# Kernel optimization log

Hardware: AMD Instinct MI355X
Metric: run time of the kernel (lower is better)

## Reference

```python
import jax, jax.numpy as jnp
import numpy as np

H, D, HID = 16, 128, 2048
B, S = 2, 2048
NUM_BLOCKS, BLOCK_SIZE = 32, 128


def _rope(x, cos, sin):
    # x: [T, H, D]; cos/sin: [T, D/2] (neox / rotate-half style)
    half = x.shape[-1] // 2
    x1, x2 = x[..., :half], x[..., half:]
    c = cos[:, None, :]
    s = sin[:, None, :]
    return jnp.concatenate([x1 * c - x2 * s, x2 * c + x1 * s], axis=-1)


def setup_inputs() -> dict:
    key = jax.random.key(0)
    ks = jax.random.split(key, 6)
    T = B * S
    hidden_states = jax.random.normal(ks[0], (T, HID), jnp.float32)
    wqkv = jax.random.normal(ks[1], (HID, 3 * HID), jnp.float32) * 0.02
    bqkv = jax.random.normal(ks[2], (3 * HID,), jnp.float32) * 0.02
    wo = jax.random.normal(ks[3], (HID, HID), jnp.float32) * 0.02
    # rotary tables, base 10000, dim = head_size
    inv_freq = 1.0 / (10000.0 ** (jnp.arange(0, D, 2, dtype=jnp.float32) / D))  # [D/2]
    pos = jnp.tile(jnp.arange(S, dtype=jnp.float32), B)  # positions per token [T]
    ang = pos[:, None] * inv_freq[None, :]  # [T, D/2]
    cos, sin = jnp.cos(ang), jnp.sin(ang)
    k_cache = jnp.zeros((NUM_BLOCKS, BLOCK_SIZE, H, D), jnp.float32)
    v_cache = jnp.zeros((NUM_BLOCKS, BLOCK_SIZE, H, D), jnp.float32)
    cu_seqlen_prefill = jnp.array([0, S, 2 * S], jnp.int32)
    slots = jnp.arange(T, dtype=jnp.int32)
    return {"hidden_states": hidden_states, "cos": cos, "sin": sin,
            "wqkv": wqkv, "bqkv": bqkv, "wo": wo,
            "k_cache": k_cache, "v_cache": v_cache,
            "cu_seqlen_prefill": cu_seqlen_prefill, "slots": slots, "max_s": S}


def reference(hidden_states, cos, sin, wqkv, bqkv, wo, k_cache, v_cache,
              cu_seqlen_prefill, slots, max_s):
    T = hidden_states.shape[0]
    # fused QKV projection (c_attn)
    qkv = hidden_states @ wqkv + bqkv  # [T, 3*H*D]
    q, k, v = jnp.split(qkv, [H * D, 2 * H * D], axis=1)
    q = q.reshape(T, H, D)
    k = k.reshape(T, H, D)
    v = v.reshape(T, H, D)
    # rotary embedding on q and k (in-place in torch; functional here)
    q = _rope(q, cos, sin)
    k = _rope(k, cos, sin)
    # reshape_and_cache: scatter post-rope k and v into paged KV cache by slot
    kc = k_cache.reshape(-1, H, D).at[slots].set(k).reshape(k_cache.shape)
    vc = v_cache.reshape(-1, H, D).at[slots].set(v).reshape(v_cache.shape)
    # prefill flash attention: varlen causal; equal-length sequences here
    b, s = T // max_s, max_s
    qb = q.reshape(b, s, H, D)
    kb = k.reshape(b, s, H, D)
    vb = v.reshape(b, s, H, D)
    scale = D ** -0.5
    scores = jnp.einsum('bqhd,bkhd->bhqk', qb, kb) * scale  # [B,H,S,S]
    causal = jnp.tril(jnp.ones((s, s), bool))
    scores = jnp.where(causal[None, None], scores, jnp.finfo(scores.dtype).min)
    probs = jax.nn.softmax(scores, axis=-1)
    attn = jnp.einsum('bhqk,bkhd->bqhd', probs, vb).reshape(T, H * D)
    out = attn @ wo  # c_proj, no bias
    return out, kc, vc
```

## Files before the change

kernel.cpp:

```cpp
#include <hip/hip_runtime.h>

using f32x4  = __attribute__((ext_vector_type(4))) float;
using frag16 = __attribute__((ext_vector_type(8))) short;
using s16x4  = __attribute__((ext_vector_type(4))) short;
using s16x8  = __attribute__((ext_vector_type(8))) short;
using u32x4  = __attribute__((ext_vector_type(4))) unsigned;

#define DI __device__ __forceinline__

constexpr int HID  = 2048;
constexpr int NH   = 16;
constexpr int HD   = 128;
constexpr int TT   = 4096;
constexpr int SEQ  = 2048;
constexpr int NQKV = 3 * HID;

DI short f2bf(float f) {
  unsigned u = __builtin_bit_cast(unsigned, f);
  unsigned r = (u + 0x7fffu + ((u >> 16) & 1u)) >> 16;
  return (short)r;
}
DI float bf2f(short s) {
  unsigned u = ((unsigned)(unsigned short)s) << 16;
  return __builtin_bit_cast(float, u);
}
DI unsigned cvtpk(float lo, float hi) {
  unsigned r;
  asm("v_cvt_pk_bf16_f32 %0, %1, %2" : "=v"(r) : "v"(lo), "v"(hi));
  return r;
}

struct alignas(8) S4h { short a, b, c, d; };

__global__ void conv_f32_bf16(const float* __restrict__ in, short* __restrict__ out) {
  int gid = blockIdx.x * 256 + threadIdx.x;
  const float4* in4 = (const float4*)in;
  float4 v = in4[gid];
  S4h o{f2bf(v.x), f2bf(v.y), f2bf(v.z), f2bf(v.w)};
  ((S4h*)out)[gid] = o;
}

template <bool IN_F32, bool PERM>
__global__ void transpose_conv(const void* __restrict__ in_, short* __restrict__ out,
                               int ldin, int R) {
  __shared__ float t[64][65];
  const float* inf = (const float*)in_;
  const short* ins = (const short*)in_;
  int tid = threadIdx.x;
  int bx = blockIdx.x, by = blockIdx.y;
#pragma unroll
  for (int i = 0; i < 4; i++) {
    int idx = i * 256 + tid;
    int r = idx >> 4, c4 = idx & 15;
    size_t gi = (size_t)(by * 64 + r) * ldin + bx * 64 + c4 * 4;
    if (IN_F32) {
      float4 v = *(const float4*)(inf + gi);
      t[r][c4 * 4] = v.x; t[r][c4 * 4 + 1] = v.y;
      t[r][c4 * 4 + 2] = v.z; t[r][c4 * 4 + 3] = v.w;
    } else {
      s16x4 v = *(const s16x4*)(ins + gi);
#pragma unroll
      for (int j = 0; j < 4; j++) t[r][c4 * 4 + j] = bf2f(v[j]);
    }
  }
  __syncthreads();
#pragma unroll
  for (int i = 0; i < 4; i++) {
    int idx = i * 256 + tid;
    int r = idx >> 4, c4 = idx & 15;
    s16x4 o;
#pragma unroll
    for (int j = 0; j < 4; j++) {
      int c = c4 * 4 + j;
      int cs = PERM ? (16 * (c & 3) + 4 * (c >> 4) + ((c >> 2) & 3)) : c;
      o[j] = f2bf(t[cs][r]);
    }
    *(s16x4*)(out + (size_t)(bx * 64 + r) * R + by * 64 + c4 * 4) = o;
  }
}

#define GLDS(src, dst)                                                     \
  __builtin_amdgcn_global_load_lds(                                        \
      (const __attribute__((address_space(1))) void*)(src),                \
      (__attribute__((address_space(3))) void*)(dst), 16, 0, 0)

template <bool ADD_BIAS, bool OUT_BF16>
__global__ __launch_bounds__(256, 2) void gemm_bt(
    const short* __restrict__ A, const short* __restrict__ Bt,
    const float* __restrict__ bias, void* __restrict__ Cout,
    int M, int N, int K) {
  __shared__ alignas(16) short Al[128 * 64];
  __shared__ alignas(16) short Bl[128 * 64];
  const int tid = threadIdx.x;
  const int wid = tid >> 6, lane = tid & 63;
  const int wr = wid >> 1, wc = wid & 1;
  const int l15 = lane & 15, lg = lane >> 4;
  const int gx = gridDim.x;
  const int id = blockIdx.y * gx + blockIdx.x;
  const int nwg = gx * gridDim.y;
  const int swz = (id & 7) * (nwg >> 3) + (id >> 3);
  const int row0 = (swz / gx) * 128, col0 = (swz % gx) * 128;
  const int lr8 = lane >> 3, l7 = lane & 7;

  f32x4 acc[4][4];
#pragma unroll
  for (int i = 0; i < 4; i++)
#pragma unroll
    for (int j = 0; j < 4; j++) acc[i][j] = {0.f, 0.f, 0.f, 0.f};

  for (int kt = 0; kt < K; kt += 64) {
#pragma unroll
    for (int c = 0; c < 4; c++) {
      int chunk = c * 4 + wid;
      int r = chunk * 8 + lr8;
      int ke = (l7 * 8) ^ ((r & 7) * 8);
      GLDS(A + (size_t)(row0 + r) * K + kt + ke, Al + chunk * 512);
      GLDS(Bt + (size_t)(col0 + r) * K + kt + ke, Bl + chunk * 512);
    }
    __syncthreads();
#pragma unroll
    for (int kk = 0; kk < 2; kk++) {
      frag16 af[4], bfv[4];
#pragma unroll
      for (int ai = 0; ai < 4; ai++) {
        int r = wr * 64 + ai * 16 + l15;
        int k0 = kk * 32 + lg * 8;
        af[ai] = *(const frag16*)(Al + r * 64 + (k0 ^ ((r & 7) * 8)));
      }
#pragma unroll
      for (int bj = 0; bj < 4; bj++) {
        int r = wc * 64 + bj * 16 + l15;
        int k0 = kk * 32 + lg * 8;
        bfv[bj] = *(const frag16*)(Bl + r * 64 + (k0 ^ ((r & 7) * 8)));
      }
#pragma unroll
      for (int ai = 0; ai < 4; ai++)
#pragma unroll
        for (int bj = 0; bj < 4; bj++)
          acc[ai][bj] = __builtin_amdgcn_mfma_f32_16x16x32_bf16(
              af[ai], bfv[bj], acc[ai][bj], 0, 0, 0);
    }
    __syncthreads();
  }
#pragma unroll
  for (int ai = 0; ai < 4; ai++) {
#pragma unroll
    for (int bj = 0; bj < 4; bj++) {
      int row = row0 + wr * 64 + ai * 16 + lg * 4;
      int col = col0 + wc * 64 + bj * 16 + l15;
      float bv = 0.f;
      if (ADD_BIAS) bv = bias[col];
#pragma unroll
      for (int r = 0; r < 4; r++) {
        float v = acc[ai][bj][r] + bv;
        if (OUT_BF16)
          ((short*)Cout)[(size_t)(row + r) * N + col] = f2bf(v);
        else
          ((float*)Cout)[(size_t)(row + r) * N + col] = v;
      }
    }
  }
}

__global__ void rope_scatter(const short* __restrict__ qkv, const float* __restrict__ cs,
                             const float* __restrict__ sn, const int* __restrict__ slots,
                             short* __restrict__ Qb, short* __restrict__ Kb,
                             float* __restrict__ kc, float* __restrict__ vc) {
  const float SCL = 0.08838834764831845f * 1.4426950408889634f;
  const int t = blockIdx.x;
  const int tid = threadIdx.x;
  const int slot = slots[t];
  const short* row = qkv + (size_t)t * NQKV;
  short* qo = Qb + (size_t)t * HID;
  short* ko = Kb + (size_t)t * HID;
  float* kco = kc + (size_t)slot * HID;
  float* vco = vc + (size_t)slot * HID;

  const int h = tid >> 4, d0 = (tid & 15) * 4;
  const int c1 = h * 128 + d0, c2 = c1 + 64;
  float4 c4 = *(const float4*)(cs + (size_t)t * 64 + d0);
  float4 s4 = *(const float4*)(sn + (size_t)t * 64 + d0);
  float cc[4] = {c4.x, c4.y, c4.z, c4.w};
  float ssv[4] = {s4.x, s4.y, s4.z, s4.w};
  s16x4 q1 = *(const s16x4*)(row + c1);
  s16x4 q2 = *(const s16x4*)(row + c2);
  s16x4 k1 = *(const s16x4*)(row + HID + c1);
  s16x4 k2 = *(const s16x4*)(row + HID + c2);
  s16x4 qo1, qo2, ko1, ko2;
  float kcv1[4], kcv2[4];
#pragma unroll
  for (int r = 0; r < 4; r++) {
    float a = bf2f(q1[r]), b = bf2f(q2[r]);
    qo1[r] = f2bf((a * cc[r] - b * ssv[r]) * SCL);
    qo2[r] = f2bf((b * cc[r] + a * ssv[r]) * SCL);
    float ka = bf2f(k1[r]), kb = bf2f(k2[r]);
    float o1 = ka * cc[r] - kb * ssv[r];
    float o2 = kb * cc[r] + ka * ssv[r];
    ko1[r] = f2bf(o1);
    ko2[r] = f2bf(o2);
    kcv1[r] = o1;
    kcv2[r] = o2;
  }
  *(s16x4*)(qo + c1) = qo1;
  *(s16x4*)(qo + c2) = qo2;
  *(s16x4*)(ko + c1) = ko1;
  *(s16x4*)(ko + c2) = ko2;
  *(float4*)(kco + c1) = {kcv1[0], kcv1[1], kcv1[2], kcv1[3]};
  *(float4*)(kco + c2) = {kcv2[0], kcv2[1], kcv2[2], kcv2[3]};

  const int vi = tid * 8;
  s16x8 v8 = *(const s16x8*)(row + 2 * HID + vi);
  *(float4*)(vco + vi)     = {bf2f(v8[0]), bf2f(v8[1]), bf2f(v8[2]), bf2f(v8[3])};
  *(float4*)(vco + vi + 4) = {bf2f(v8[4]), bf2f(v8[5]), bf2f(v8[6]), bf2f(v8[7])};
}

__global__ __launch_bounds__(256, 2) void flash_attn5(
    const short* __restrict__ Qb, const short* __restrict__ Kb,
    const short* __restrict__ Vt, short* __restrict__ attn) {
  __shared__ alignas(16) short Klds[2][64 * 128];
  __shared__ alignas(16) short Vlds[2][128 * 64];
  __shared__ alignas(16) short plds[4][16 * 72];

  const int tid = threadIdx.x;
  const int w = tid >> 6, lane = tid & 63;
  const int l15 = lane & 15, lg = lane >> 4;
  const int bid = blockIdx.x;
  const int p = bid >> 5;
  const int bh = bid & 31;
  const int b = bh >> 4, h = bh & 15;
  short* pl = &plds[w][0];

  frag16 ones;
#pragma unroll
  for (int j = 0; j < 8; j++) ones[j] = (short)0x3F80;

  auto stage = [&](int kv0, int buf) {
#pragma unroll
    for (int ci = 0; ci < 4; ci++) {
      int cc = w * 4 + ci;
      int krow = cc * 4 + (lane >> 4);
      int kss = (lane & 15) ^ (krow & 15);
      GLDS(Kb + (size_t)(b * SEQ + kv0 + krow) * HID + h * HD + kss * 8,
           Klds[buf] + cc * 512);
      int vd = cc * 8 + (lane >> 3);
      int vss = (lane & 7) ^ (vd & 7);
      GLDS(Vt + (size_t)(h * HD + vd) * TT + b * SEQ + kv0 + vss * 8,
           Vlds[buf] + cc * 512);
    }
  };

  const int qrowH = (31 - p) * 64 + w * 16;
  const int qrowL = p * 64 + w * 16;
  const int ntH = 32 - p;

  frag16 qfH[4], qfL[4];
  {
    const short* qpH = Qb + (size_t)(b * SEQ + qrowH + l15) * HID + h * HD + lg * 8;
    const short* qpL = Qb + (size_t)(b * SEQ + qrowL + l15) * HID + h * HD + lg * 8;
#pragma unroll
    for (int ds = 0; ds < 4; ds++) {
      qfH[ds] = *(const frag16*)(qpH + ds * 32);
      qfL[ds] = *(const frag16*)(qpL + ds * 32);
    }
  }
  f32x4 oH[8], oL[8];
#pragma unroll
  for (int j = 0; j < 8; j++) { oH[j] = {0.f, 0.f, 0.f, 0.f}; oL[j] = {0.f, 0.f, 0.f, 0.f}; }
  f32x4 laH = {0.f, 0.f, 0.f, 0.f}, laL = {0.f, 0.f, 0.f, 0.f};
  float mrH = -1e30f, mrL = -1e30f;

  auto proc = [&](const frag16 (&qf)[4], f32x4 (&o)[8], f32x4& la, float& mr,
                  bool diag, const short* Kl, const short* Vl) {
    f32x4 sa[4];
#pragma unroll
    for (int f = 0; f < 4; f++) sa[f] = {0.f, 0.f, 0.f, 0.f};
#pragma unroll
    for (int ds = 0; ds < 4; ds++) {
      int phys = (ds * 4 + lg) ^ l15;
#pragma unroll
      for (int f = 0; f < 4; f++) {
        frag16 kf = *(const frag16*)(Kl + (f * 16 + l15) * 128 + phys * 8);
        sa[f] = __builtin_amdgcn_mfma_f32_16x16x32_bf16(kf, qf[ds], sa[f], 0, 0, 0);
      }
    }
    if (diag) {
      int ql = 16 * w + l15;
#pragma unroll
      for (int f = 0; f < 4; f++)
#pragma unroll
        for (int r = 0; r < 4; r++)
          if (f * 16 + lg * 4 + r > ql) sa[f][r] = -1e30f;
    }
    float pm = sa[0][0];
#pragma unroll
    for (int f = 0; f < 4; f++)
#pragma unroll
      for (int r = 0; r < 4; r++) pm = fmaxf(pm, sa[f][r]);
    pm = fmaxf(pm, __shfl_xor(pm, 16));
    pm = fmaxf(pm, __shfl_xor(pm, 32));
    if (__any(pm > mr + 8.f)) {
      float mn = fmaxf(mr, pm);
      float frl = exp2f(mr - mn);
      mr = mn;
      float fr4[4];
#pragma unroll
      for (int r = 0; r < 4; r++)
        fr4[r] = __shfl(frl, lg * 16 + lg * 4 + r);
#pragma unroll
      for (int r = 0; r < 4; r++) {
        la[r] *= fr4[r];
#pragma unroll
        for (int j = 0; j < 8; j++) o[j][r] *= fr4[r];
      }
    }
    float pe[4][4];
#pragma unroll
    for (int f = 0; f < 4; f++)
#pragma unroll
      for (int r = 0; r < 4; r++) pe[f][r] = exp2f(sa[f][r] - mr);
    unsigned wv[8];
#pragma unroll
    for (int r = 0; r < 4; r++) {
      wv[2 * r]     = cvtpk(pe[0][r], pe[1][r]);
      wv[2 * r + 1] = cvtpk(pe[2][r], pe[3][r]);
    }
    {
      u32x4* pb = (u32x4*)(pl + l15 * 72 + lg * 16);
      pb[0] = {wv[0], wv[1], wv[2], wv[3]};
      pb[1] = {wv[4], wv[5], wv[6], wv[7]};
    }
    asm volatile("s_waitcnt lgkmcnt(0)" ::: "memory");
    frag16 pf0 = *(const frag16*)(pl + l15 * 72 + lg * 8);
    frag16 pf1 = *(const frag16*)(pl + l15 * 72 + 32 + lg * 8);
    la = __builtin_amdgcn_mfma_f32_16x16x32_bf16(pf0, ones, la, 0, 0, 0);
    la = __builtin_amdgcn_mfma_f32_16x16x32_bf16(pf1, ones, la, 0, 0, 0);
#pragma unroll
    for (int j = 0; j < 8; j++) {
      int d = j * 16 + l15;
      int p0 = lg ^ (d & 7);
      int p1 = (4 + lg) ^ (d & 7);
      frag16 vf0 = *(const frag16*)(Vl + d * 64 + p0 * 8);
      frag16 vf1 = *(const frag16*)(Vl + d * 64 + p1 * 8);
      o[j] = __builtin_amdgcn_mfma_f32_16x16x32_bf16(pf0, vf0, o[j], 0, 0, 0);
      o[j] = __builtin_amdgcn_mfma_f32_16x16x32_bf16(pf1, vf1, o[j], 0, 0, 0);
    }
  };

  stage(0, 0);
  __syncthreads();

  int cur = 0;
  for (int t = 0; t < ntH; t++) {
    if (t + 1 < ntH) stage((t + 1) * 64, cur ^ 1);
    const short* Kl = &Klds[cur][0];
    const short* Vl = &Vlds[cur][0];
    proc(qfH, oH, laH, mrH, t == ntH - 1, Kl, Vl);
    if (t <= p) proc(qfL, oL, laL, mrL, t == p, Kl, Vl);
    __syncthreads();
    cur ^= 1;
  }

  {
    float inv[4];
#pragma unroll
    for (int r = 0; r < 4; r++) inv[r] = 1.f / laH[r];
    short* op = attn + (size_t)(b * SEQ + qrowH + lg * 4) * HID + h * HD + l15;
#pragma unroll
    for (int j = 0; j < 8; j++)
#pragma unroll
      for (int r = 0; r < 4; r++)
        op[(size_t)r * HID + j * 16] = f2bf(oH[j][r] * inv[r]);
  }
  {
    float inv[4];
#pragma unroll
    for (int r = 0; r < 4; r++) inv[r] = 1.f / laL[r];
    short* op = attn + (size_t)(b * SEQ + qrowL + lg * 4) * HID + h * HD + l15;
#pragma unroll
    for (int j = 0; j < 8; j++)
#pragma unroll
      for (int r = 0; r < 4; r++)
        op[(size_t)r * HID + j * 16] = f2bf(oL[j][r] * inv[r]);
  }
}

extern "C" void kernel_launch(void* const* d_in, const int* in_sizes, int n_in,
                              void* d_out, int out_size, void* d_ws, size_t ws_size,
                              hipStream_t stream) {
  const float* hidden = (const float*)d_in[0];
  const float* cosb   = (const float*)d_in[1];
  const float* sinb   = (const float*)d_in[2];
  const float* wqkv   = (const float*)d_in[3];
  const float* bqkv   = (const float*)d_in[4];
  const float* wo     = (const float*)d_in[5];
  const int*   slots  = (const int*)d_in[9];

  float* out = (float*)d_out;
  float* kc  = out + (size_t)TT * HID;
  float* vc  = kc + (size_t)TT * HID;

  short* ws    = (short*)d_ws;
  short* Abf   = ws;
  short* Wqkvt = Abf + 8388608;
  short* Wot   = Wqkvt + 12582912;
  short* qkvb  = Wot + 4194304;
  short* Qb    = qkvb + 25165824;
  short* Kb    = Qb + 8388608;
  short* Vt    = Kb + 8388608;
  short* attnb = Abf;

  conv_f32_bf16<<<8192, 256, 0, stream>>>(hidden, Abf);
  transpose_conv<true, false><<<dim3(96, 32), 256, 0, stream>>>(wqkv, Wqkvt, NQKV, HID);
  transpose_conv<true, false><<<dim3(32, 32), 256, 0, stream>>>(wo, Wot, HID, HID);
  gemm_bt<true, true><<<dim3(48, 32), 256, 0, stream>>>(Abf, Wqkvt, bqkv, qkvb,
                                                        TT, NQKV, HID);
  rope_scatter<<<TT, 256, 0, stream>>>(qkvb, cosb, sinb, slots, Qb, Kb, kc, vc);
  transpose_conv<false, true><<<dim3(32, 64), 256, 0, stream>>>(qkvb + 2 * HID, Vt, NQKV, TT);
  flash_attn5<<<512, 256, 0, stream>>>(Qb, Kb, Vt, attnb);
  gemm_bt<false, false><<<dim3(16, 32), 256, 0, stream>>>(attnb, Wot, nullptr, out,
                                                          TT, HID, HID);
}
```

Before: 291.8 us.

## Fuse RoPE, KV-cache scatter and V transpose into QKV GEMM epilogue

The QKV GEMM epilogue now applies bias and RoPE, writes Q/K in bf16, scatters K/V into the fp32 caches, and writes V transposed and permuted for flash attention. This removes the bf16 qkv intermediate round trip and two separate kernels (rope_scatter, V transpose). The B-fragment column mapping is remapped so each wave holds d and d+64 pairs for the rotation. The epilogue stores become scattered scalar writes, notably the strided Vt stores. Separately, s_setprio hints are added around the MFMA blocks in flash attention.

```diff
diff --git a/kernel.cpp b/kernel.cpp
--- a/kernel.cpp
+++ b/kernel.cpp
@@ -14,6 +14,7 @@
 constexpr int TT   = 4096;
 constexpr int SEQ  = 2048;
 constexpr int NQKV = 3 * HID;
+constexpr float SCL = 0.08838834764831845f * 1.4426950408889634f;
 
 DI short f2bf(float f) {
   unsigned u = __builtin_bit_cast(unsigned, f);
@@ -40,12 +41,9 @@
   ((S4h*)out)[gid] = o;
 }
 
-template <bool IN_F32, bool PERM>
-__global__ void transpose_conv(const void* __restrict__ in_, short* __restrict__ out,
+__global__ void transpose_conv(const float* __restrict__ in, short* __restrict__ out,
                                int ldin, int R) {
   __shared__ float t[64][65];
-  const float* inf = (const float*)in_;
-  const short* ins = (const short*)in_;
   int tid = threadIdx.x;
   int bx = blockIdx.x, by = blockIdx.y;
 #pragma unroll
@@ -53,15 +51,9 @@
     int idx = i * 256 + tid;
     int r = idx >> 4, c4 = idx & 15;
     size_t gi = (size_t)(by * 64 + r) * ldin + bx * 64 + c4 * 4;
-    if (IN_F32) {
-      float4 v = *(const float4*)(inf + gi);
-      t[r][c4 * 4] = v.x; t[r][c4 * 4 + 1] = v.y;
-      t[r][c4 * 4 + 2] = v.z; t[r][c4 * 4 + 3] = v.w;
-    } else {
-      s16x4 v = *(const s16x4*)(ins + gi);
-#pragma unroll
-      for (int j = 0; j < 4; j++) t[r][c4 * 4 + j] = bf2f(v[j]);
-    }
+    float4 v = *(const float4*)(in + gi);
+    t[r][c4 * 4] = v.x; t[r][c4 * 4 + 1] = v.y;
+    t[r][c4 * 4 + 2] = v.z; t[r][c4 * 4 + 3] = v.w;
   }
   __syncthreads();
 #pragma unroll
@@ -70,11 +62,7 @@
     int r = idx >> 4, c4 = idx & 15;
     s16x4 o;
 #pragma unroll
-    for (int j = 0; j < 4; j++) {
-      int c = c4 * 4 + j;
-      int cs = PERM ? (16 * (c & 3) + 4 * (c >> 4) + ((c >> 2) & 3)) : c;
-      o[j] = f2bf(t[cs][r]);
-    }
+    for (int j = 0; j < 4; j++) o[j] = f2bf(t[c4 * 4 + j][r]);
     *(s16x4*)(out + (size_t)(bx * 64 + r) * R + by * 64 + c4 * 4) = o;
   }
 }
@@ -84,10 +72,14 @@
       (const __attribute__((address_space(1))) void*)(src),                \
       (__attribute__((address_space(3))) void*)(dst), 16, 0, 0)
 
-template <bool ADD_BIAS, bool OUT_BF16>
+template <int EPI>
 __global__ __launch_bounds__(256, 2) void gemm_bt(
     const short* __restrict__ A, const short* __restrict__ Bt,
-    const float* __restrict__ bias, void* __restrict__ Cout,
+    const float* __restrict__ bias, float* __restrict__ Cout,
+    const float* __restrict__ cs, const float* __restrict__ sn,
+    const int* __restrict__ slots,
+    short* __restrict__ Qb, short* __restrict__ Kb, short* __restrict__ Vt,
+    float* __restrict__ kc, float* __restrict__ vc,
     int M, int N, int K) {
   __shared__ alignas(16) short Al[128 * 64];
   __shared__ alignas(16) short Bl[128 * 64];
@@ -129,7 +121,7 @@
       }
 #pragma unroll
       for (int bj = 0; bj < 4; bj++) {
-        int r = wc * 64 + bj * 16 + l15;
+        int r = wc * 16 + (bj & 1) * 32 + ((bj >> 1) << 6) + l15;
         int k0 = kk * 32 + lg * 8;
         bfv[bj] = *(const frag16*)(Bl + r * 64 + (k0 ^ ((r & 7) * 8)));
       }
@@ -142,76 +134,60 @@
     }
     __syncthreads();
   }
-#pragma unroll
-  for (int ai = 0; ai < 4; ai++) {
-#pragma unroll
-    for (int bj = 0; bj < 4; bj++) {
-      int row = row0 + wr * 64 + ai * 16 + lg * 4;
-      int col = col0 + wc * 64 + bj * 16 + l15;
-      float bv = 0.f;
-      if (ADD_BIAS) bv = bias[col];
-#pragma unroll
-      for (int r = 0; r < 4; r++) {
-        float v = acc[ai][bj][r] + bv;
-        if (OUT_BF16)
-          ((short*)Cout)[(size_t)(row + r) * N + col] = f2bf(v);
-        else
-          ((float*)Cout)[(size_t)(row + r) * N + col] = v;
-      }
-    }
-  }
-}
-
-__global__ void rope_scatter(const short* __restrict__ qkv, const float* __restrict__ cs,
-                             const float* __restrict__ sn, const int* __restrict__ slots,
-                             short* __restrict__ Qb, short* __restrict__ Kb,
-                             float* __restrict__ kc, float* __restrict__ vc) {
-  const float SCL = 0.08838834764831845f * 1.4426950408889634f;
-  const int t = blockIdx.x;
-  const int tid = threadIdx.x;
-  const int slot = slots[t];
-  const short* row = qkv + (size_t)t * NQKV;
-  short* qo = Qb + (size_t)t * HID;
-  short* ko = Kb + (size_t)t * HID;
-  float* kco = kc + (size_t)slot * HID;
-  float* vco = vc + (size_t)slot * HID;
-
-  const int h = tid >> 4, d0 = (tid & 15) * 4;
-  const int c1 = h * 128 + d0, c2 = c1 + 64;
-  float4 c4 = *(const float4*)(cs + (size_t)t * 64 + d0);
-  float4 s4 = *(const float4*)(sn + (size_t)t * 64 + d0);
-  float cc[4] = {c4.x, c4.y, c4.z, c4.w};
-  float ssv[4] = {s4.x, s4.y, s4.z, s4.w};
-  s16x4 q1 = *(const s16x4*)(row + c1);
-  s16x4 q2 = *(const s16x4*)(row + c2);
-  s16x4 k1 = *(const s16x4*)(row + HID + c1);
-  s16x4 k2 = *(const s16x4*)(row + HID + c2);
-  s16x4 qo1, qo2, ko1, ko2;
-  float kcv1[4], kcv2[4];
-#pragma unroll
-  for (int r = 0; r < 4; r++) {
-    float a = bf2f(q1[r]), b = bf2f(q2[r]);
-    qo1[r] = f2bf((a * cc[r] - b * ssv[r]) * SCL);
-    qo2[r] = f2bf((b * cc[r] + a * ssv[r]) * SCL);
-    float ka = bf2f(k1[r]), kb = bf2f(k2[r]);
-    float o1 = ka * cc[r] - kb * ssv[r];
-    float o2 = kb * cc[r] + ka * ssv[r];
-    ko1[r] = f2bf(o1);
-    ko2[r] = f2bf(o2);
-    kcv1[r] = o1;
-    kcv2[r] = o2;
-  }
-  *(s16x4*)(qo + c1) = qo1;
-  *(s16x4*)(qo + c2) = qo2;
-  *(s16x4*)(ko + c1) = ko1;
-  *(s16x4*)(ko + c2) = ko2;
-  *(float4*)(kco + c1) = {kcv1[0], kcv1[1], kcv1[2], kcv1[3]};
-  *(float4*)(kco + c2) = {kcv2[0], kcv2[1], kcv2[2], kcv2[3]};
-
-  const int vi = tid * 8;
-  s16x8 v8 = *(const s16x8*)(row + 2 * HID + vi);
-  *(float4*)(vco + vi)     = {bf2f(v8[0]), bf2f(v8[1]), bf2f(v8[2]), bf2f(v8[3])};
-  *(float4*)(vco + vi + 4) = {bf2f(v8[4]), bf2f(v8[5]), bf2f(v8[6]), bf2f(v8[7])};
+
+  if (EPI == 0) {
+#pragma unroll
+    for (int ai = 0; ai < 4; ai++) {
+#pragma unroll
+      for (int bj = 0; bj < 4; bj++) {
+        int row = row0 + wr * 64 + ai * 16 + lg * 4;
+        int col = col0 + wc * 16 + (bj & 1) * 32 + ((bj >> 1) << 6) + l15;
+#pragma unroll
+        for (int r = 0; r < 4; r++)
+          Cout[(size_t)(row + r) * N + col] = acc[ai][bj][r];
+      }
+    }
+  } else {
+    const int sec = col0 >> 11;
+    const int h = (col0 & 2047) >> 7;
+#pragma unroll
+    for (int ai = 0; ai < 4; ai++) {
+#pragma unroll
+      for (int bj = 0; bj < 2; bj++) {
+        const int d1 = wc * 16 + bj * 32 + l15;
+        const float b1 = bias[col0 + d1];
+        const float b2 = bias[col0 + d1 + 64];
+        const int base = h * 128 + d1;
+#pragma unroll
+        for (int r = 0; r < 4; r++) {
+          const int tok = row0 + wr * 64 + ai * 16 + lg * 4 + r;
+          float v1 = acc[ai][bj][r] + b1;
+          float v2 = acc[ai][bj + 2][r] + b2;
+          if (sec == 0) {
+            float c = cs[tok * 64 + d1], s = sn[tok * 64 + d1];
+            Qb[(size_t)tok * HID + base]      = f2bf((v1 * c - v2 * s) * SCL);
+            Qb[(size_t)tok * HID + base + 64] = f2bf((v2 * c + v1 * s) * SCL);
+          } else if (sec == 1) {
+            float c = cs[tok * 64 + d1], s = sn[tok * 64 + d1];
+            float o1 = v1 * c - v2 * s, o2 = v2 * c + v1 * s;
+            int sl = slots[tok];
+            Kb[(size_t)tok * HID + base]      = f2bf(o1);
+            Kb[(size_t)tok * HID + base + 64] = f2bf(o2);
+            kc[(size_t)sl * HID + base]      = o1;
+            kc[(size_t)sl * HID + base + 64] = o2;
+          } else {
+            int sl = slots[tok];
+            vc[(size_t)sl * HID + base]      = v1;
+            vc[(size_t)sl * HID + base + 64] = v2;
+            int tsub = tok & 63;
+            int cp = (tok & ~63) + 16 * ((tsub >> 2) & 3) + 4 * (tsub & 3) + (tsub >> 4);
+            Vt[(size_t)base * TT + cp]        = f2bf(v1);
+            Vt[(size_t)(base + 64) * TT + cp] = f2bf(v2);
+          }
+        }
+      }
+    }
+  }
 }
 
 __global__ __launch_bounds__(256, 2) void flash_attn5(
@@ -274,6 +250,7 @@
     f32x4 sa[4];
 #pragma unroll
     for (int f = 0; f < 4; f++) sa[f] = {0.f, 0.f, 0.f, 0.f};
+    __builtin_amdgcn_s_setprio(1);
 #pragma unroll
     for (int ds = 0; ds < 4; ds++) {
       int phys = (ds * 4 + lg) ^ l15;
@@ -283,6 +260,7 @@
         sa[f] = __builtin_amdgcn_mfma_f32_16x16x32_bf16(kf, qf[ds], sa[f], 0, 0, 0);
       }
     }
+    __builtin_amdgcn_s_setprio(0);
     if (diag) {
       int ql = 16 * w + l15;
 #pragma unroll
@@ -332,6 +310,7 @@
     asm volatile("s_waitcnt lgkmcnt(0)" ::: "memory");
     frag16 pf0 = *(const frag16*)(pl + l15 * 72 + lg * 8);
     frag16 pf1 = *(const frag16*)(pl + l15 * 72 + 32 + lg * 8);
+    __builtin_amdgcn_s_setprio(1);
     la = __builtin_amdgcn_mfma_f32_16x16x32_bf16(pf0, ones, la, 0, 0, 0);
     la = __builtin_amdgcn_mfma_f32_16x16x32_bf16(pf1, ones, la, 0, 0, 0);
 #pragma unroll
@@ -344,6 +323,7 @@
       o[j] = __builtin_amdgcn_mfma_f32_16x16x32_bf16(pf0, vf0, o[j], 0, 0, 0);
       o[j] = __builtin_amdgcn_mfma_f32_16x16x32_bf16(pf1, vf1, o[j], 0, 0, 0);
     }
+    __builtin_amdgcn_s_setprio(0);
   };
 
   stage(0, 0);
@@ -403,20 +383,19 @@
   short* Abf   = ws;
   short* Wqkvt = Abf + 8388608;
   short* Wot   = Wqkvt + 12582912;
-  short* qkvb  = Wot + 4194304;
-  short* Qb    = qkvb + 25165824;
+  short* Qb    = Wot + 4194304;
   short* Kb    = Qb + 8388608;
   short* Vt    = Kb + 8388608;
   short* attnb = Abf;
 
   conv_f32_bf16<<<8192, 256, 0, stream>>>(hidden, Abf);
-  transpose_conv<true, false><<<dim3(96, 32), 256, 0, stream>>>(wqkv, Wqkvt, NQKV, HID);
-  transpose_conv<true, false><<<dim3(32, 32), 256, 0, stream>>>(wo, Wot, HID, HID);
-  gemm_bt<true, true><<<dim3(48, 32), 256, 0, stream>>>(Abf, Wqkvt, bqkv, qkvb,
-                                                        TT, NQKV, HID);
-  rope_scatter<<<TT, 256, 0, stream>>>(qkvb, cosb, sinb, slots, Qb, Kb, kc, vc);
-  transpose_conv<false, true><<<dim3(32, 64), 256, 0, stream>>>(qkvb + 2 * HID, Vt, NQKV, TT);
+  transpose_conv<<<dim3(96, 32), 256, 0, stream>>>(wqkv, Wqkvt, NQKV, HID);
+  transpose_conv<<<dim3(32, 32), 256, 0, stream>>>(wo, Wot, HID, HID);
+  gemm_bt<1><<<dim3(48, 32), 256, 0, stream>>>(
+      Abf, Wqkvt, bqkv, nullptr, cosb, sinb, slots, Qb, Kb, Vt, kc, vc,
+      TT, NQKV, HID);
   flash_attn5<<<512, 256, 0, stream>>>(Qb, Kb, Vt, attnb);
-  gemm_bt<false, false><<<dim3(16, 32), 256, 0, stream>>>(attnb, Wot, nullptr, out,
-                                                          TT, HID, HID);
-}
+  gemm_bt<0><<<dim3(16, 32), 256, 0, stream>>>(
+      attnb, Wot, nullptr, out, nullptr, nullptr, nullptr,
+      nullptr, nullptr, nullptr, nullptr, nullptr, TT, HID, HID);
+}
```

Result: no change. 295.3 us (+1.2%).

## Double-buffer GEMM with 8-wave 128x256 tiles and raise MFMA priority

Applied to the files above, without the earlier changes.

Replaces the single-buffered 4-wave 128x128 GEMM with an 8-wave kernel that computes 128x256 output tiles. It stages K tiles into double-buffered dynamic LDS using global_load_lds, with vmcnt waits and raw barriers, so loads of the next tile overlap MFMA work on the current one. It also wraps MFMA blocks in s_setprio in both the GEMM and the flash attention kernel to favour the matrix pipe. The cost is 96KB of LDS per block (occupancy limits) and fewer workgroups in the out-projection GEMM (256 blocks).

```diff
diff --git a/kernel.cpp b/kernel.cpp
--- a/kernel.cpp
+++ b/kernel.cpp
@@ -14,6 +14,7 @@
 constexpr int TT   = 4096;
 constexpr int SEQ  = 2048;
 constexpr int NQKV = 3 * HID;
+constexpr float SCL = 0.08838834764831845f * 1.4426950408889634f;
 
 DI short f2bf(float f) {
   unsigned u = __builtin_bit_cast(unsigned, f);
@@ -84,23 +85,23 @@
       (const __attribute__((address_space(1))) void*)(src),                \
       (__attribute__((address_space(3))) void*)(dst), 16, 0, 0)
 
+#define BARRIER asm volatile("s_barrier" ::: "memory")
+
 template <bool ADD_BIAS, bool OUT_BF16>
-__global__ __launch_bounds__(256, 2) void gemm_bt(
+__global__ __launch_bounds__(512, 2) void gemm8p(
     const short* __restrict__ A, const short* __restrict__ Bt,
     const float* __restrict__ bias, void* __restrict__ Cout,
     int M, int N, int K) {
-  __shared__ alignas(16) short Al[128 * 64];
-  __shared__ alignas(16) short Bl[128 * 64];
+  extern __shared__ short smem[];
   const int tid = threadIdx.x;
   const int wid = tid >> 6, lane = tid & 63;
-  const int wr = wid >> 1, wc = wid & 1;
+  const int wrm = wid >> 2, wcn = wid & 3;
   const int l15 = lane & 15, lg = lane >> 4;
   const int gx = gridDim.x;
   const int id = blockIdx.y * gx + blockIdx.x;
   const int nwg = gx * gridDim.y;
   const int swz = (id & 7) * (nwg >> 3) + (id >> 3);
-  const int row0 = (swz / gx) * 128, col0 = (swz % gx) * 128;
-  const int lr8 = lane >> 3, l7 = lane & 7;
+  const int row0 = (swz / gx) * 128, col0 = (swz % gx) * 256;
 
   f32x4 acc[4][4];
 #pragma unroll
@@ -108,51 +109,73 @@
 #pragma unroll
     for (int j = 0; j < 4; j++) acc[i][j] = {0.f, 0.f, 0.f, 0.f};
 
-  for (int kt = 0; kt < K; kt += 64) {
-#pragma unroll
-    for (int c = 0; c < 4; c++) {
-      int chunk = c * 4 + wid;
-      int r = chunk * 8 + lr8;
-      int ke = (l7 * 8) ^ ((r & 7) * 8);
-      GLDS(A + (size_t)(row0 + r) * K + kt + ke, Al + chunk * 512);
-      GLDS(Bt + (size_t)(col0 + r) * K + kt + ke, Bl + chunk * 512);
-    }
-    __syncthreads();
+  auto stage = [&](int kt, int nb) {
+    short* Ad = smem + nb * 24576;
+    short* Bd = Ad + 8192;
+#pragma unroll
+    for (int g = 0; g < 2; g++) {
+      int idx = g * 512 + tid;
+      int row = idx >> 3;
+      int ke = ((idx & 7) ^ (row & 7)) * 8;
+      GLDS(A + (size_t)(row0 + row) * K + kt + ke, Ad + (g * 512 + wid * 64) * 8);
+    }
+#pragma unroll
+    for (int g = 0; g < 4; g++) {
+      int idx = g * 512 + tid;
+      int row = idx >> 3;
+      int ke = ((idx & 7) ^ (row & 7)) * 8;
+      GLDS(Bt + (size_t)(col0 + row) * K + kt + ke, Bd + (g * 512 + wid * 64) * 8);
+    }
+  };
+
+  const int NT = K >> 6;
+  stage(0, 0);
+
+  for (int t = 0; t < NT; ++t) {
+    const int cur = t & 1;
+    const short* Ab = smem + cur * 24576;
+    const short* Bb = Ab + 8192;
+    if (t + 1 < NT) {
+      stage((t + 1) << 6, cur ^ 1);
+      asm volatile("s_waitcnt vmcnt(6)" ::: "memory");
+    } else {
+      asm volatile("s_waitcnt vmcnt(0)" ::: "memory");
+    }
+    BARRIER;
 #pragma unroll
     for (int kk = 0; kk < 2; kk++) {
-      frag16 af[4], bfv[4];
-#pragma unroll
-      for (int ai = 0; ai < 4; ai++) {
-        int r = wr * 64 + ai * 16 + l15;
-        int k0 = kk * 32 + lg * 8;
-        af[ai] = *(const frag16*)(Al + r * 64 + (k0 ^ ((r & 7) * 8)));
+      frag16 af[4], bf[4];
+#pragma unroll
+      for (int i = 0; i < 4; i++) {
+        int ra = wrm * 64 + i * 16 + l15;
+        af[i] = *(const frag16*)(Ab + ra * 64 + (((kk * 4 + lg) ^ (ra & 7)) * 8));
+        int rb = wcn * 64 + i * 16 + l15;
+        bf[i] = *(const frag16*)(Bb + rb * 64 + (((kk * 4 + lg) ^ (rb & 7)) * 8));
       }
-#pragma unroll
-      for (int bj = 0; bj < 4; bj++) {
-        int r = wc * 64 + bj * 16 + l15;
-        int k0 = kk * 32 + lg * 8;
-        bfv[bj] = *(const frag16*)(Bl + r * 64 + (k0 ^ ((r & 7) * 8)));
-      }
-#pragma unroll
-      for (int ai = 0; ai < 4; ai++)
-#pragma unroll
-        for (int bj = 0; bj < 4; bj++)
-          acc[ai][bj] = __builtin_amdgcn_mfma_f32_16x16x32_bf16(
-              af[ai], bfv[bj], acc[ai][bj], 0, 0, 0);
-    }
-    __syncthreads();
-  }
-#pragma unroll
-  for (int ai = 0; ai < 4; ai++) {
-#pragma unroll
-    for (int bj = 0; bj < 4; bj++) {
-      int row = row0 + wr * 64 + ai * 16 + lg * 4;
-      int col = col0 + wc * 64 + bj * 16 + l15;
+      BARRIER;
+      __builtin_amdgcn_s_setprio(1);
+#pragma unroll
+      for (int i = 0; i < 4; i++)
+#pragma unroll
+        for (int j = 0; j < 4; j++)
+          acc[i][j] = __builtin_amdgcn_mfma_f32_16x16x32_bf16(
+              af[i], bf[j], acc[i][j], 0, 0, 0);
+      __builtin_amdgcn_s_setprio(0);
+      BARRIER;
+    }
+  }
+
+#pragma unroll
+  for (int i = 0; i < 4; i++) {
+#pragma unroll
+    for (int j = 0; j < 4; j++) {
+      int row = row0 + wrm * 64 + i * 16 + lg * 4;
+      int col = col0 + wcn * 64 + j * 16 + l15;
       float bv = 0.f;
       if (ADD_BIAS) bv = bias[col];
 #pragma unroll
       for (int r = 0; r < 4; r++) {
-        float v = acc[ai][bj][r] + bv;
+        float v = acc[i][j][r] + bv;
         if (OUT_BF16)
           ((short*)Cout)[(size_t)(row + r) * N + col] = f2bf(v);
         else
@@ -166,7 +189,6 @@
                              const float* __restrict__ sn, const int* __restrict__ slots,
                              short* __restrict__ Qb, short* __restrict__ Kb,
                              float* __restrict__ kc, float* __restrict__ vc) {
-  const float SCL = 0.08838834764831845f * 1.4426950408889634f;
   const int t = blockIdx.x;
   const int tid = threadIdx.x;
   const int slot = slots[t];
@@ -274,6 +296,7 @@
     f32x4 sa[4];
 #pragma unroll
     for (int f = 0; f < 4; f++) sa[f] = {0.f, 0.f, 0.f, 0.f};
+    __builtin_amdgcn_s_setprio(1);
 #pragma unroll
     for (int ds = 0; ds < 4; ds++) {
       int phys = (ds * 4 + lg) ^ l15;
@@ -283,6 +306,7 @@
         sa[f] = __builtin_amdgcn_mfma_f32_16x16x32_bf16(kf, qf[ds], sa[f], 0, 0, 0);
       }
     }
+    __builtin_amdgcn_s_setprio(0);
     if (diag) {
       int ql = 16 * w + l15;
 #pragma unroll
@@ -332,6 +356,7 @@
     asm volatile("s_waitcnt lgkmcnt(0)" ::: "memory");
     frag16 pf0 = *(const frag16*)(pl + l15 * 72 + lg * 8);
     frag16 pf1 = *(const frag16*)(pl + l15 * 72 + 32 + lg * 8);
+    __builtin_amdgcn_s_setprio(1);
     la = __builtin_amdgcn_mfma_f32_16x16x32_bf16(pf0, ones, la, 0, 0, 0);
     la = __builtin_amdgcn_mfma_f32_16x16x32_bf16(pf1, ones, la, 0, 0, 0);
 #pragma unroll
@@ -344,6 +369,7 @@
       o[j] = __builtin_amdgcn_mfma_f32_16x16x32_bf16(pf0, vf0, o[j], 0, 0, 0);
       o[j] = __builtin_amdgcn_mfma_f32_16x16x32_bf16(pf1, vf1, o[j], 0, 0, 0);
     }
+    __builtin_amdgcn_s_setprio(0);
   };
 
   stage(0, 0);
@@ -409,14 +435,19 @@
   short* Vt    = Kb + 8388608;
   short* attnb = Abf;
 
+  hipFuncSetAttribute(reinterpret_cast<const void*>(&gemm8p<true, true>),
+                      hipFuncAttributeMaxDynamicSharedMemorySize, 98304);
+  hipFuncSetAttribute(reinterpret_cast<const void*>(&gemm8p<false, false>),
+                      hipFuncAttributeMaxDynamicSharedMemorySize, 98304);
+
   conv_f32_bf16<<<8192, 256, 0, stream>>>(hidden, Abf);
   transpose_conv<true, false><<<dim3(96, 32), 256, 0, stream>>>(wqkv, Wqkvt, NQKV, HID);
   transpose_conv<true, false><<<dim3(32, 32), 256, 0, stream>>>(wo, Wot, HID, HID);
-  gemm_bt<true, true><<<dim3(48, 32), 256, 0, stream>>>(Abf, Wqkvt, bqkv, qkvb,
-                                                        TT, NQKV, HID);
+  gemm8p<true, true><<<dim3(24, 32), 512, 98304, stream>>>(
+      Abf, Wqkvt, bqkv, qkvb, TT, NQKV, HID);
   rope_scatter<<<TT, 256, 0, stream>>>(qkvb, cosb, sinb, slots, Qb, Kb, kc, vc);
   transpose_conv<false, true><<<dim3(32, 64), 256, 0, stream>>>(qkvb + 2 * HID, Vt, NQKV, TT);
   flash_attn5<<<512, 256, 0, stream>>>(Qb, Kb, Vt, attnb);
-  gemm_bt<false, false><<<dim3(16, 32), 256, 0, stream>>>(attnb, Wot, nullptr, out,
-                                                          TT, HID, HID);
-}
+  gemm8p<false, false><<<dim3(8, 32), 512, 98304, stream>>>(
+      attnb, Wot, nullptr, out, TT, HID, HID);
+}
```

New measurement: 293.2 us. About the same (+0.5%).
